# Kernel optimization log

Hardware: AMD Instinct MI355X
Metric: run time of the kernel (lower is better)

The kernel has to match this reference:

```python
import jax, jax.numpy as jnp
import numpy as np

DIM = 1536
DSTATE = 16


def setup_inputs() -> dict:
    key = jax.random.key(0)
    ks = jax.random.split(key, 8)
    batch, dim, seqlen, dstate = 4, DIM, 4096, DSTATE
    u = jax.random.normal(ks[0], (batch, dim, seqlen), dtype=jnp.float32)
    delta = jax.random.uniform(ks[1], (batch, dim, seqlen), dtype=jnp.float32)
    B = jax.random.normal(ks[2], (batch, dstate, seqlen), dtype=jnp.float32)
    C = jax.random.normal(ks[3], (batch, dstate, seqlen), dtype=jnp.float32)
    A = -jnp.exp(jax.random.normal(ks[4], (dim, dstate), dtype=jnp.float32))
    D = jax.random.normal(ks[5], (dim,), dtype=jnp.float32)
    delta_bias = jax.random.normal(ks[6], (dim,), dtype=jnp.float32)
    return {"u": u, "delta": delta, "B": B, "C": C, "A": A, "D": D, "delta_bias": delta_bias}


def _selective_scan(u, delta, B, C, A, D, delta_bias):
    # u, delta: [b, d, s]; B, C: [b, n, s]; A: [d, n]; D, delta_bias: [d]
    dt = jax.nn.softplus(delta + delta_bias[None, :, None])  # [b, d, s]
    # scan over time: carry x [b, d, n]
    dt_s = jnp.moveaxis(dt, 2, 0)   # [s, b, d]
    u_s = jnp.moveaxis(u, 2, 0)     # [s, b, d]
    B_s = jnp.moveaxis(B, 2, 0)     # [s, b, n]
    C_s = jnp.moveaxis(C, 2, 0)     # [s, b, n]

    def step(x, inp):
        dt_t, u_t, B_t, C_t = inp  # [b,d], [b,d], [b,n], [b,n]
        dA = jnp.exp(dt_t[..., None] * A[None])           # [b, d, n]
        dBu = (dt_t * u_t)[..., None] * B_t[:, None, :]   # [b, d, n]
        x = dA * x + dBu
        y = jnp.einsum('bdn,bn->bd', x, C_t) + D[None] * u_t
        return x, y

    b, d, s = u.shape
    n = A.shape[1]
    x0 = jnp.zeros((b, d, n), dtype=jnp.float32)
    _, ys = jax.lax.scan(step, x0, (dt_s, u_s, B_s, C_s))  # ys: [s, b, d]
    return jnp.moveaxis(ys, 0, 2)  # [b, d, s]


def reference(u, delta, B, C, A, D, delta_bias):
    return _selective_scan(u, delta, B, C, A, D, delta_bias)
```

## Files before the change

kernel.cpp:

```cpp
#include <hip/hip_runtime.h>

#define BATCH 4
#define DIM   1536
#define SEQ   4096
#define NST   16
#define NCHAN (BATCH*DIM)
#define NCH   32
#define CLEN  128
#define T     16
#define LBSTR 20

#define LOG2E 1.4426950408889634f

__device__ __forceinline__ float softplus_f(float z) {
    return (z > 20.f) ? z : __logf(1.f + __expf(z));
}
__device__ __forceinline__ float exp2_hw(float z) {
    return __builtin_amdgcn_exp2f(z);
}

template<int CTRL>
__device__ __forceinline__ float dpp_qp(float v) {
    return __int_as_float(
        __builtin_amdgcn_mov_dpp(__float_as_int(v), CTRL, 0xf, 0xf, true));
}
__device__ __forceinline__ float quad_sum(float v) {
    v += dpp_qp<0xB1>(v);
    v += dpp_qp<0x4E>(v);
    return v;
}


__global__ __launch_bounds__(256, 6) void ssm_phaseA(
    const float* __restrict__ u, const float* __restrict__ delta,
    const float* __restrict__ Bm, const float* __restrict__ A,
    const float* __restrict__ dbias,
    float* __restrict__ sumdt_out, float* __restrict__ S_out)
{
    __shared__ float lB[4 * T * LBSTR];

    const int tid = threadIdx.x;
    const int w   = tid >> 6;
    const int l   = tid & 63;
    const int q   = l >> 2;
    const int sub = l & 3;
    const int cj  = sub << 2;

    const int ch0 = blockIdx.x * 64;
    const int ch  = ch0 + w * 16 + q;
    const int d   = ch % DIM;
    const int bb  = ch0 / DIM;
    const int k   = blockIdx.y;
    const int s0  = k * CLEN;

    float* LB = &lB[w * T * LBSTR];

    float A2[4];
    {
        const float4 av = *(const float4*)(A + (size_t)d * NST + sub * 4);
        A2[0] = av.x * LOG2E; A2[1] = av.y * LOG2E;
        A2[2] = av.z * LOG2E; A2[3] = av.w * LOG2E;
    }
    const float sbias = dbias[d];

    const size_t ubase = (size_t)ch * SEQ + s0;
    const size_t bbase = ((size_t)bb * NST + q) * SEQ + s0;

    float4 run = *(const float4*)(u + ubase + cj);
    float4 rdn = *(const float4*)(delta + ubase + cj);
    float4 rbn = *(const float4*)(Bm + bbase + cj);

    float S[4] = {0.f, 0.f, 0.f, 0.f};
    float sumdt = 0.f;

    for (int ss = 0; ss < CLEN; ss += T) {
        const float uc[4] = {run.x, run.y, run.z, run.w};
        const float dc[4] = {softplus_f(rdn.x + sbias), softplus_f(rdn.y + sbias),
                             softplus_f(rdn.z + sbias), softplus_f(rdn.w + sbias)};
        sumdt += (dc[0] + dc[1]) + (dc[2] + dc[3]);

        LB[(cj + 0) * LBSTR + q] = rbn.x;
        LB[(cj + 1) * LBSTR + q] = rbn.y;
        LB[(cj + 2) * LBSTR + q] = rbn.z;
        LB[(cj + 3) * LBSTR + q] = rbn.w;

        if (ss + T < CLEN) {
            run = *(const float4*)(u + ubase + (ss + T) + cj);
            rdn = *(const float4*)(delta + ubase + (ss + T) + cj);
            rbn = *(const float4*)(Bm + bbase + (ss + T) + cj);
        }

#define ASTEP(ii) { \
        const float dt  = dpp_qp<(((ii) >> 2) * 0x55)>(dc[(ii) & 3]); \
        const float uu  = dpp_qp<(((ii) >> 2) * 0x55)>(uc[(ii) & 3]); \
        const float dtu = dt * uu; \
        const float4 bv = *(const float4*)(&LB[(ii) * LBSTR + cj]); \
        S[0] = fmaf(exp2_hw(dt * A2[0]), S[0], dtu * bv.x); \
        S[1] = fmaf(exp2_hw(dt * A2[1]), S[1], dtu * bv.y); \
        S[2] = fmaf(exp2_hw(dt * A2[2]), S[2], dtu * bv.z); \
        S[3] = fmaf(exp2_hw(dt * A2[3]), S[3], dtu * bv.w); \
    }
        ASTEP(0)  ASTEP(1)  ASTEP(2)  ASTEP(3)
        ASTEP(4)  ASTEP(5)  ASTEP(6)  ASTEP(7)
        ASTEP(8)  ASTEP(9)  ASTEP(10) ASTEP(11)
        ASTEP(12) ASTEP(13) ASTEP(14) ASTEP(15)
#undef ASTEP
    }

    *(float4*)(S_out + ((size_t)k * NCHAN + ch) * NST + sub * 4) =
        make_float4(S[0], S[1], S[2], S[3]);

    const float sfull = quad_sum(sumdt);
    if (sub == 0) sumdt_out[(size_t)k * NCHAN + ch] = sfull;
}

__global__ __launch_bounds__(256) void ssm_phaseB(
    const float* __restrict__ A, const float* __restrict__ sumdt,
    float* __restrict__ S)
{
    const int t  = blockIdx.x * 256 + threadIdx.x;
    const int n  = t & 15;
    const int ch = t >> 4;
    if (ch >= NCHAN) return;
    const int d = ch % DIM;
    const float An2 = A[(size_t)d * NST + n] * LOG2E;

    const size_t kstride = (size_t)NCHAN * NST;
    size_t idx = (size_t)ch * NST + n;

    float x = 0.f;
    float s_nxt = S[idx];
    float p_nxt = sumdt[ch];
#pragma unroll 4
    for (int k = 0; k < NCH; k++) {
        const float s_old = s_nxt;
        const float pdt   = p_nxt;
        if (k + 1 < NCH) {
            s_nxt = S[idx + kstride];
            p_nxt = sumdt[(size_t)(k + 1) * NCHAN + ch];
        }
        S[idx] = x;
        x = fmaf(exp2_hw(An2 * pdt), x, s_old);
        idx += kstride;
    }
}

__global__ __launch_bounds__(256, 6) void ssm_phaseC(
    const float* __restrict__ u, const float* __restrict__ delta,
    const float* __restrict__ Bm, const float* __restrict__ Cm,
    const float* __restrict__ A, const float* __restrict__ Dv,
    const float* __restrict__ dbias, const float* __restrict__ x0,
    float* __restrict__ y)
{
    __shared__ float lB[4 * T * LBSTR];
    __shared__ float lC[4 * T * LBSTR];

    const int tid = threadIdx.x;
    const int w   = tid >> 6;
    const int l   = tid & 63;
    const int q   = l >> 2;
    const int sub = l & 3;
    const int cj  = sub << 2;

    const int ch0 = blockIdx.x * 64;
    const int ch  = ch0 + w * 16 + q;
    const int d   = ch % DIM;
    const int bb  = ch0 / DIM;
    const int k   = blockIdx.y;
    const int s0  = k * CLEN;

    float* LB = &lB[w * T * LBSTR];
    float* LC = &lC[w * T * LBSTR];

    float A2[4];
    {
        const float4 av = *(const float4*)(A + (size_t)d * NST + sub * 4);
        A2[0] = av.x * LOG2E; A2[1] = av.y * LOG2E;
        A2[2] = av.z * LOG2E; A2[3] = av.w * LOG2E;
    }
    const float sbias = dbias[d];
    const float Dval  = Dv[d];

    float x[4];
    {
        const float4 xv = *(const float4*)(x0 + ((size_t)k * NCHAN + ch) * NST + sub * 4);
        x[0] = xv.x; x[1] = xv.y; x[2] = xv.z; x[3] = xv.w;
    }

    const size_t ubase = (size_t)ch * SEQ + s0;
    const size_t bbase = ((size_t)bb * NST + q) * SEQ + s0;

    float4 run = *(const float4*)(u + ubase + cj);
    float4 rdn = *(const float4*)(delta + ubase + cj);
    float4 rbn = *(const float4*)(Bm + bbase + cj);
    float4 rcn = *(const float4*)(Cm + bbase + cj);

    for (int ss = 0; ss < CLEN; ss += T) {
        const float uc[4] = {run.x, run.y, run.z, run.w};
        const float dc[4] = {softplus_f(rdn.x + sbias), softplus_f(rdn.y + sbias),
                             softplus_f(rdn.z + sbias), softplus_f(rdn.w + sbias)};

        LB[(cj + 0) * LBSTR + q] = rbn.x;
        LB[(cj + 1) * LBSTR + q] = rbn.y;
        LB[(cj + 2) * LBSTR + q] = rbn.z;
        LB[(cj + 3) * LBSTR + q] = rbn.w;
        LC[(cj + 0) * LBSTR + q] = rcn.x;
        LC[(cj + 1) * LBSTR + q] = rcn.y;
        LC[(cj + 2) * LBSTR + q] = rcn.z;
        LC[(cj + 3) * LBSTR + q] = rcn.w;

        if (ss + T < CLEN) {
            run = *(const float4*)(u + ubase + (ss + T) + cj);
            rdn = *(const float4*)(delta + ubase + (ss + T) + cj);
            rbn = *(const float4*)(Bm + bbase + (ss + T) + cj);
            rcn = *(const float4*)(Cm + bbase + (ss + T) + cj);
        }

        float yreg[4];

#define CSTEP(ii) { \
        const float dt  = dpp_qp<(((ii) >> 2) * 0x55)>(dc[(ii) & 3]); \
        const float uu  = dpp_qp<(((ii) >> 2) * 0x55)>(uc[(ii) & 3]); \
        const float dtu = dt * uu; \
        const float4 bv = *(const float4*)(&LB[(ii) * LBSTR + cj]); \
        const float4 cv = *(const float4*)(&LC[(ii) * LBSTR + cj]); \
        x[0] = fmaf(exp2_hw(dt * A2[0]), x[0], dtu * bv.x); \
        x[1] = fmaf(exp2_hw(dt * A2[1]), x[1], dtu * bv.y); \
        x[2] = fmaf(exp2_hw(dt * A2[2]), x[2], dtu * bv.z); \
        x[3] = fmaf(exp2_hw(dt * A2[3]), x[3], dtu * bv.w); \
        float acc = x[0] * cv.x; \
        acc = fmaf(x[1], cv.y, acc); \
        acc = fmaf(x[2], cv.z, acc); \
        acc = fmaf(x[3], cv.w, acc); \
        acc = quad_sum(acc); \
        const float yv = fmaf(Dval, uu, acc); \
        if (sub == ((ii) >> 2)) yreg[(ii) & 3] = yv; \
    }
        CSTEP(0)  CSTEP(1)  CSTEP(2)  CSTEP(3)
        CSTEP(4)  CSTEP(5)  CSTEP(6)  CSTEP(7)
        CSTEP(8)  CSTEP(9)  CSTEP(10) CSTEP(11)
        CSTEP(12) CSTEP(13) CSTEP(14) CSTEP(15)
#undef CSTEP

        *(float4*)(y + ubase + ss + sub * 4) =
            make_float4(yreg[0], yreg[1], yreg[2], yreg[3]);
    }
}

extern "C" void kernel_launch(void* const* d_in, const int* in_sizes, int n_in,
                              void* d_out, int out_size, void* d_ws, size_t ws_size,
                              hipStream_t stream)
{
    const float* u     = (const float*)d_in[0];
    const float* delta = (const float*)d_in[1];
    const float* Bm    = (const float*)d_in[2];
    const float* Cm    = (const float*)d_in[3];
    const float* A     = (const float*)d_in[4];
    const float* Dv    = (const float*)d_in[5];
    const float* dbias = (const float*)d_in[6];
    float* y = (float*)d_out;

    float* sumdt = (float*)d_ws;
    float* S     = sumdt + (size_t)NCHAN * NCH;

    const dim3 grid(NCHAN / 64, NCH);
    ssm_phaseA<<<grid, 256, 0, stream>>>(u, delta, Bm, A, dbias, sumdt, S);
    ssm_phaseB<<<(NCHAN * NST) / 256, 256, 0, stream>>>(A, sumdt, S);
    ssm_phaseC<<<grid, 256, 0, stream>>>(u, delta, Bm, Cm, A, Dv, dbias, S, y);
}
```

Measured before the change: 537.6 us.

## Template chunk length, deepen u/delta prefetch, precompute dt*u, raise occupancy

Turns the chunk length into a template parameter and picks 64-step chunks when the workspace is large enough, which doubles the number of chunks so there are more blocks. The u and delta loads get a three-deep register ring buffer that prefetches two tiles ahead, and dt*u is computed once per element and broadcast with a single DPP instead of two. In phase C the D*u term moves out of the per-step quad reduction into one float4 update before the store, and launch bounds rise from 6 to 8 waves. In exchange, the phase-B serial scan and the workspace traffic double in length, and the larger register ring may press against the tighter register limit.

```diff
diff --git a/kernel.cpp b/kernel.cpp
--- a/kernel.cpp
+++ b/kernel.cpp
@@ -5,8 +5,6 @@
 #define SEQ   4096
 #define NST   16
 #define NCHAN (BATCH*DIM)
-#define NCH   32
-#define CLEN  128
 #define T     16
 #define LBSTR 20
 
@@ -31,12 +29,14 @@
 }
 
 
-__global__ __launch_bounds__(256, 6) void ssm_phaseA(
+template<int CLEN>
+__global__ __launch_bounds__(256, 8) void ssm_phaseA(
     const float* __restrict__ u, const float* __restrict__ delta,
     const float* __restrict__ Bm, const float* __restrict__ A,
     const float* __restrict__ dbias,
     float* __restrict__ sumdt_out, float* __restrict__ S_out)
 {
+    constexpr int NT = CLEN / T;
     __shared__ float lB[4 * T * LBSTR];
 
     const int tid = threadIdx.x;
@@ -57,7 +57,7 @@
 
     float A2[4];
     {
-        const float4 av = *(const float4*)(A + (size_t)d * NST + sub * 4);
+        const float4 av = *(const float4*)(A + (size_t)d * NST + cj);
         A2[0] = av.x * LOG2E; A2[1] = av.y * LOG2E;
         A2[2] = av.z * LOG2E; A2[3] = av.w * LOG2E;
     }
@@ -66,34 +66,42 @@
     const size_t ubase = (size_t)ch * SEQ + s0;
     const size_t bbase = ((size_t)bb * NST + q) * SEQ + s0;
 
-    float4 run = *(const float4*)(u + ubase + cj);
-    float4 rdn = *(const float4*)(delta + ubase + cj);
-    float4 rbn = *(const float4*)(Bm + bbase + cj);
+    float4 PU[3], PD[3], RB;
+    PU[0] = *(const float4*)(u + ubase + cj);
+    PD[0] = *(const float4*)(delta + ubase + cj);
+    PU[1] = *(const float4*)(u + ubase + T + cj);
+    PD[1] = *(const float4*)(delta + ubase + T + cj);
+    RB = *(const float4*)(Bm + bbase + cj);
 
     float S[4] = {0.f, 0.f, 0.f, 0.f};
     float sumdt = 0.f;
 
-    for (int ss = 0; ss < CLEN; ss += T) {
-        const float uc[4] = {run.x, run.y, run.z, run.w};
-        const float dc[4] = {softplus_f(rdn.x + sbias), softplus_f(rdn.y + sbias),
-                             softplus_f(rdn.z + sbias), softplus_f(rdn.w + sbias)};
+#pragma unroll
+    for (int t = 0; t < NT; ++t) {
+        const int cb = t % 3;
+        const int ss = t * T;
+
+        LB[(cj + 0) * LBSTR + q] = RB.x;
+        LB[(cj + 1) * LBSTR + q] = RB.y;
+        LB[(cj + 2) * LBSTR + q] = RB.z;
+        LB[(cj + 3) * LBSTR + q] = RB.w;
+
+        if (t + 1 < NT)
+            RB = *(const float4*)(Bm + bbase + (ss + T) + cj);
+        if (t + 2 < NT) {
+            PU[(t + 2) % 3] = *(const float4*)(u + ubase + (ss + 2 * T) + cj);
+            PD[(t + 2) % 3] = *(const float4*)(delta + ubase + (ss + 2 * T) + cj);
+        }
+
+        const float dc[4] = {softplus_f(PD[cb].x + sbias), softplus_f(PD[cb].y + sbias),
+                             softplus_f(PD[cb].z + sbias), softplus_f(PD[cb].w + sbias)};
+        const float du[4] = {dc[0] * PU[cb].x, dc[1] * PU[cb].y,
+                             dc[2] * PU[cb].z, dc[3] * PU[cb].w};
         sumdt += (dc[0] + dc[1]) + (dc[2] + dc[3]);
-
-        LB[(cj + 0) * LBSTR + q] = rbn.x;
-        LB[(cj + 1) * LBSTR + q] = rbn.y;
-        LB[(cj + 2) * LBSTR + q] = rbn.z;
-        LB[(cj + 3) * LBSTR + q] = rbn.w;
-
-        if (ss + T < CLEN) {
-            run = *(const float4*)(u + ubase + (ss + T) + cj);
-            rdn = *(const float4*)(delta + ubase + (ss + T) + cj);
-            rbn = *(const float4*)(Bm + bbase + (ss + T) + cj);
-        }
 
 #define ASTEP(ii) { \
         const float dt  = dpp_qp<(((ii) >> 2) * 0x55)>(dc[(ii) & 3]); \
-        const float uu  = dpp_qp<(((ii) >> 2) * 0x55)>(uc[(ii) & 3]); \
-        const float dtu = dt * uu; \
+        const float dtu = dpp_qp<(((ii) >> 2) * 0x55)>(du[(ii) & 3]); \
         const float4 bv = *(const float4*)(&LB[(ii) * LBSTR + cj]); \
         S[0] = fmaf(exp2_hw(dt * A2[0]), S[0], dtu * bv.x); \
         S[1] = fmaf(exp2_hw(dt * A2[1]), S[1], dtu * bv.y); \
@@ -107,13 +115,14 @@
 #undef ASTEP
     }
 
-    *(float4*)(S_out + ((size_t)k * NCHAN + ch) * NST + sub * 4) =
+    *(float4*)(S_out + ((size_t)k * NCHAN + ch) * NST + cj) =
         make_float4(S[0], S[1], S[2], S[3]);
 
     const float sfull = quad_sum(sumdt);
     if (sub == 0) sumdt_out[(size_t)k * NCHAN + ch] = sfull;
 }
 
+template<int NCH>
 __global__ __launch_bounds__(256) void ssm_phaseB(
     const float* __restrict__ A, const float* __restrict__ sumdt,
     float* __restrict__ S)
@@ -145,13 +154,15 @@
     }
 }
 
-__global__ __launch_bounds__(256, 6) void ssm_phaseC(
+template<int CLEN>
+__global__ __launch_bounds__(256, 8) void ssm_phaseC(
     const float* __restrict__ u, const float* __restrict__ delta,
     const float* __restrict__ Bm, const float* __restrict__ Cm,
     const float* __restrict__ A, const float* __restrict__ Dv,
     const float* __restrict__ dbias, const float* __restrict__ x0,
     float* __restrict__ y)
 {
+    constexpr int NT = CLEN / T;
     __shared__ float lB[4 * T * LBSTR];
     __shared__ float lC[4 * T * LBSTR];
 
@@ -174,7 +185,7 @@
 
     float A2[4];
     {
-        const float4 av = *(const float4*)(A + (size_t)d * NST + sub * 4);
+        const float4 av = *(const float4*)(A + (size_t)d * NST + cj);
         A2[0] = av.x * LOG2E; A2[1] = av.y * LOG2E;
         A2[2] = av.z * LOG2E; A2[3] = av.w * LOG2E;
     }
@@ -183,45 +194,54 @@
 
     float x[4];
     {
-        const float4 xv = *(const float4*)(x0 + ((size_t)k * NCHAN + ch) * NST + sub * 4);
+        const float4 xv = *(const float4*)(x0 + ((size_t)k * NCHAN + ch) * NST + cj);
         x[0] = xv.x; x[1] = xv.y; x[2] = xv.z; x[3] = xv.w;
     }
 
     const size_t ubase = (size_t)ch * SEQ + s0;
     const size_t bbase = ((size_t)bb * NST + q) * SEQ + s0;
 
-    float4 run = *(const float4*)(u + ubase + cj);
-    float4 rdn = *(const float4*)(delta + ubase + cj);
-    float4 rbn = *(const float4*)(Bm + bbase + cj);
-    float4 rcn = *(const float4*)(Cm + bbase + cj);
-
-    for (int ss = 0; ss < CLEN; ss += T) {
-        const float uc[4] = {run.x, run.y, run.z, run.w};
-        const float dc[4] = {softplus_f(rdn.x + sbias), softplus_f(rdn.y + sbias),
-                             softplus_f(rdn.z + sbias), softplus_f(rdn.w + sbias)};
-
-        LB[(cj + 0) * LBSTR + q] = rbn.x;
-        LB[(cj + 1) * LBSTR + q] = rbn.y;
-        LB[(cj + 2) * LBSTR + q] = rbn.z;
-        LB[(cj + 3) * LBSTR + q] = rbn.w;
-        LC[(cj + 0) * LBSTR + q] = rcn.x;
-        LC[(cj + 1) * LBSTR + q] = rcn.y;
-        LC[(cj + 2) * LBSTR + q] = rcn.z;
-        LC[(cj + 3) * LBSTR + q] = rcn.w;
-
-        if (ss + T < CLEN) {
-            run = *(const float4*)(u + ubase + (ss + T) + cj);
-            rdn = *(const float4*)(delta + ubase + (ss + T) + cj);
-            rbn = *(const float4*)(Bm + bbase + (ss + T) + cj);
-            rcn = *(const float4*)(Cm + bbase + (ss + T) + cj);
+    float4 PU[3], PD[3], RB, RC;
+    PU[0] = *(const float4*)(u + ubase + cj);
+    PD[0] = *(const float4*)(delta + ubase + cj);
+    PU[1] = *(const float4*)(u + ubase + T + cj);
+    PD[1] = *(const float4*)(delta + ubase + T + cj);
+    RB = *(const float4*)(Bm + bbase + cj);
+    RC = *(const float4*)(Cm + bbase + cj);
+
+#pragma unroll
+    for (int t = 0; t < NT; ++t) {
+        const int cb = t % 3;
+        const int ss = t * T;
+
+        LB[(cj + 0) * LBSTR + q] = RB.x;
+        LB[(cj + 1) * LBSTR + q] = RB.y;
+        LB[(cj + 2) * LBSTR + q] = RB.z;
+        LB[(cj + 3) * LBSTR + q] = RB.w;
+        LC[(cj + 0) * LBSTR + q] = RC.x;
+        LC[(cj + 1) * LBSTR + q] = RC.y;
+        LC[(cj + 2) * LBSTR + q] = RC.z;
+        LC[(cj + 3) * LBSTR + q] = RC.w;
+
+        if (t + 1 < NT) {
+            RB = *(const float4*)(Bm + bbase + (ss + T) + cj);
+            RC = *(const float4*)(Cm + bbase + (ss + T) + cj);
         }
+        if (t + 2 < NT) {
+            PU[(t + 2) % 3] = *(const float4*)(u + ubase + (ss + 2 * T) + cj);
+            PD[(t + 2) % 3] = *(const float4*)(delta + ubase + (ss + 2 * T) + cj);
+        }
+
+        const float dc[4] = {softplus_f(PD[cb].x + sbias), softplus_f(PD[cb].y + sbias),
+                             softplus_f(PD[cb].z + sbias), softplus_f(PD[cb].w + sbias)};
+        const float du[4] = {dc[0] * PU[cb].x, dc[1] * PU[cb].y,
+                             dc[2] * PU[cb].z, dc[3] * PU[cb].w};
 
         float yreg[4];
 
 #define CSTEP(ii) { \
         const float dt  = dpp_qp<(((ii) >> 2) * 0x55)>(dc[(ii) & 3]); \
-        const float uu  = dpp_qp<(((ii) >> 2) * 0x55)>(uc[(ii) & 3]); \
-        const float dtu = dt * uu; \
+        const float dtu = dpp_qp<(((ii) >> 2) * 0x55)>(du[(ii) & 3]); \
         const float4 bv = *(const float4*)(&LB[(ii) * LBSTR + cj]); \
         const float4 cv = *(const float4*)(&LC[(ii) * LBSTR + cj]); \
         x[0] = fmaf(exp2_hw(dt * A2[0]), x[0], dtu * bv.x); \
@@ -233,8 +253,7 @@
         acc = fmaf(x[2], cv.z, acc); \
         acc = fmaf(x[3], cv.w, acc); \
         acc = quad_sum(acc); \
-        const float yv = fmaf(Dval, uu, acc); \
-        if (sub == ((ii) >> 2)) yreg[(ii) & 3] = yv; \
+        if (sub == ((ii) >> 2)) yreg[(ii) & 3] = acc; \
     }
         CSTEP(0)  CSTEP(1)  CSTEP(2)  CSTEP(3)
         CSTEP(4)  CSTEP(5)  CSTEP(6)  CSTEP(7)
@@ -242,9 +261,29 @@
         CSTEP(12) CSTEP(13) CSTEP(14) CSTEP(15)
 #undef CSTEP
 
-        *(float4*)(y + ubase + ss + sub * 4) =
+        yreg[0] = fmaf(Dval, PU[cb].x, yreg[0]);
+        yreg[1] = fmaf(Dval, PU[cb].y, yreg[1]);
+        yreg[2] = fmaf(Dval, PU[cb].z, yreg[2]);
+        yreg[3] = fmaf(Dval, PU[cb].w, yreg[3]);
+        *(float4*)(y + ubase + ss + cj) =
             make_float4(yreg[0], yreg[1], yreg[2], yreg[3]);
     }
+}
+
+template<int CLEN>
+static void run_pipeline(const float* u, const float* delta, const float* Bm,
+                         const float* Cm, const float* A, const float* Dv,
+                         const float* dbias, float* y, float* ws,
+                         hipStream_t stream)
+{
+    constexpr int NCH = SEQ / CLEN;
+    float* sumdt = ws;
+    float* S     = ws + (size_t)NCH * NCHAN;
+
+    const dim3 grid(NCHAN / 64, NCH);
+    ssm_phaseA<CLEN><<<grid, 256, 0, stream>>>(u, delta, Bm, A, dbias, sumdt, S);
+    ssm_phaseB<NCH><<<(NCHAN * NST) / 256, 256, 0, stream>>>(A, sumdt, S);
+    ssm_phaseC<CLEN><<<grid, 256, 0, stream>>>(u, delta, Bm, Cm, A, Dv, dbias, S, y);
 }
 
 extern "C" void kernel_launch(void* const* d_in, const int* in_sizes, int n_in,
@@ -258,13 +297,13 @@
     const float* A     = (const float*)d_in[4];
     const float* Dv    = (const float*)d_in[5];
     const float* dbias = (const float*)d_in[6];
-    float* y = (float*)d_out;
-
-    float* sumdt = (float*)d_ws;
-    float* S     = sumdt + (size_t)NCHAN * NCH;
-
-    const dim3 grid(NCHAN / 64, NCH);
-    ssm_phaseA<<<grid, 256, 0, stream>>>(u, delta, Bm, A, dbias, sumdt, S);
-    ssm_phaseB<<<(NCHAN * NST) / 256, 256, 0, stream>>>(A, sumdt, S);
-    ssm_phaseC<<<grid, 256, 0, stream>>>(u, delta, Bm, Cm, A, Dv, dbias, S, y);
-}
+    float* y  = (float*)d_out;
+    float* ws = (float*)d_ws;
+
+    const size_t need64 = ((size_t)64 * NCHAN + (size_t)64 * NCHAN * NST) * sizeof(float);
+    if (ws_size >= need64) {
+        run_pipeline<64>(u, delta, Bm, Cm, A, Dv, dbias, y, ws, stream);
+    } else {
+        run_pipeline<128>(u, delta, Bm, Cm, A, Dv, dbias, y, ws, stream);
+    }
+}
```

Result: slower. 763.1 us (+41.9%).
